# Performance work log

Hardware: AMD Instinct MI355X
Metric: run time of the kernel (lower is better)

The kernel has to match this reference:

```python
import jax, jax.numpy as jnp
import numpy as np

HIDDEN = 1000
DICT = 4811
T = 44
B = 256


def _lstm_cell(x, h, c, W_ih, W_hh, b_ih, b_hh):
    # gates: [B, 4*H], PyTorch order i, f, g, o
    gates = x @ W_ih.T + b_ih + h @ W_hh.T + b_hh
    i, f, g, o = jnp.split(gates, 4, axis=-1)
    i = jax.nn.sigmoid(i)
    f = jax.nn.sigmoid(f)
    g = jnp.tanh(g)
    o = jax.nn.sigmoid(o)
    c_new = f * c + i * g
    h_new = o * jnp.tanh(c_new)
    return h_new, c_new


def setup_inputs() -> dict:
    key = jax.random.key(0)
    ks = jax.random.split(key, 20)
    s = 0.02
    H = HIDDEN
    return {
        "x": jax.random.normal(ks[0], (B, T, H), jnp.float32),
        "h1": jax.random.normal(ks[1], (B, H), jnp.float32),
        "h2": jax.random.normal(ks[2], (B, H), jnp.float32),
        "c1": jax.random.normal(ks[3], (B, H), jnp.float32),
        "c2": jax.random.normal(ks[4], (B, H), jnp.float32),
        "layer_W": jax.random.normal(ks[5], (H, H), jnp.float32) * s,
        "layer_b": jnp.zeros((H,), jnp.float32),
        "W_ih1": jax.random.normal(ks[6], (4 * H, 2 * H), jnp.float32) * s,
        "W_hh1": jax.random.normal(ks[7], (4 * H, H), jnp.float32) * s,
        "b_ih1": jnp.zeros((4 * H,), jnp.float32),
        "b_hh1": jnp.zeros((4 * H,), jnp.float32),
        "W_ih2": jax.random.normal(ks[8], (4 * H, DICT + 2 * H), jnp.float32) * s,
        "W_hh2": jax.random.normal(ks[9], (4 * H, H), jnp.float32) * s,
        "b_ih2": jnp.zeros((4 * H,), jnp.float32),
        "b_hh2": jnp.zeros((4 * H,), jnp.float32),
        "out_W": jax.random.normal(ks[10], (DICT, H), jnp.float32) * s,
        "out_b": jnp.zeros((DICT,), jnp.float32),
    }


def reference(x, h1, h2, c1, c2, layer_W, layer_b,
              W_ih1, W_hh1, b_ih1, b_hh1,
              W_ih2, W_hh2, b_ih2, b_hh2,
              out_W, out_b):
    # input projection: [B, T, H]
    xp = x @ layer_W.T + layer_b
    prev0 = jnp.zeros((x.shape[0], DICT), x.dtype)

    def step(carry, xt):
        h1, c1, h2, c2, prev = carry
        l1_in = jnp.concatenate([xt, h1], axis=1)            # [B, 2H]
        h1n, c1n = _lstm_cell(l1_in, h1, c1, W_ih1, W_hh1, b_ih1, b_hh1)
        l2_in = jnp.concatenate([prev, h2, h1n], axis=1)     # [B, DICT+2H]
        h2n, c2n = _lstm_cell(l2_in, h2, c2, W_ih2, W_hh2, b_ih2, b_hh2)
        logits = h2n @ out_W.T + out_b                       # [B, DICT]
        # NOTE: original torch code softmaxes over dim=0 (batch axis)
        y = jax.nn.softmax(logits, axis=0)
        return (h1n, c1n, h2n, c2n, y), y

    xs = jnp.transpose(xp, (1, 0, 2))                        # [T, B, H]
    _, ys = jax.lax.scan(step, (h1, c1, h2, c2, prev0), xs)
    return jnp.transpose(ys, (1, 0, 2))                      # [B, T, DICT]
```

## Files before the change

### kernel.cpp

```cpp
#include <hip/hip_runtime.h>
#include <hip/hip_bf16.h>

#define HID   1000
#define DICT  4811
#define TT    44
#define BB    256
#define G4    4000
#define G4P   4096
#define K1P   2048
#define K2P   6912
#define HP    1024
#define DP    4864
#define Z2_H2 4864
#define Z2_H1 5888

typedef __attribute__((ext_vector_type(8))) short short8;
typedef __attribute__((ext_vector_type(4))) float f32x4;

__device__ __forceinline__ short f2b(float f) {
    unsigned u = __float_as_uint(f);
    unsigned r = (u + 0x7FFFu + ((u >> 16) & 1u)) >> 16;
    return (short)r;
}

__device__ __forceinline__ void gload16(const void* g, const short* l) {
    __builtin_amdgcn_global_load_lds(
        (const __attribute__((address_space(1))) unsigned int*)g,
        (__attribute__((address_space(3))) unsigned int*)l, 16, 0, 0);
}

__global__ void prep_w1p(const float* __restrict__ wih1, const float* __restrict__ whh1,
                         short* __restrict__ w) {
    for (size_t i = (size_t)blockIdx.x * blockDim.x + threadIdx.x; i < (size_t)G4P * K1P;
         i += (size_t)gridDim.x * blockDim.x) {
        int n = (int)(i >> 11), j = (int)(i & 2047);
        float v = 0.f;
        if (n < G4) {
            if (j < HID) v = wih1[(size_t)n * 2000 + j];
            else if (j >= 1024 && j < 1024 + HID) {
                int jj = j - 1024;
                v = wih1[(size_t)n * 2000 + HID + jj] + whh1[(size_t)n * HID + jj];
            }
        }
        w[i] = f2b(v);
    }
}

__global__ void prep_w2p(const float* __restrict__ wih2, const float* __restrict__ whh2,
                         short* __restrict__ w) {
    int n = blockIdx.y;
    int j = blockIdx.x * 256 + threadIdx.x;
    float v = 0.f;
    if (n < G4) {
        if (j < DICT) v = wih2[(size_t)n * 6811 + j];
        else if (j >= Z2_H2 && j < Z2_H2 + HID) {
            int jj = j - Z2_H2;
            v = wih2[(size_t)n * 6811 + DICT + jj] + whh2[(size_t)n * HID + jj];
        } else if (j >= Z2_H1 && j < Z2_H1 + HID) {
            int jj = j - Z2_H1;
            v = wih2[(size_t)n * 6811 + DICT + HID + jj];
        }
    }
    w[(size_t)n * K2P + j] = f2b(v);
}

__global__ void prep_outwp(const float* __restrict__ outw, short* __restrict__ w) {
    int n = blockIdx.y;
    int j = blockIdx.x * 256 + threadIdx.x;
    float v = (n < DICT && j < HID) ? outw[(size_t)n * HID + j] : 0.f;
    w[(size_t)n * HP + j] = f2b(v);
}

__global__ void prep_cvt(const float* __restrict__ src, short* __restrict__ dst, size_t n) {
    for (size_t i = (size_t)blockIdx.x * blockDim.x + threadIdx.x; i < n;
         i += (size_t)gridDim.x * blockDim.x)
        dst[i] = f2b(src[i]);
}

__global__ void prep_addv(const float* __restrict__ a, const float* __restrict__ b,
                          float* __restrict__ dst, int n) {
    int i = blockIdx.x * blockDim.x + threadIdx.x;
    if (i < n) dst[i] = a[i] + b[i];
}

__global__ void init_vec(const float* __restrict__ src, short* __restrict__ dst, int ld) {
    int i = blockIdx.x * blockDim.x + threadIdx.x;
    if (i >= BB * HID) return;
    int b = i / HID, h = i % HID;
    dst[(size_t)b * ld + h] = f2b(src[i]);
}

template <int EPI, int AF32>
__global__ __launch_bounds__(256) void gemm_nt(
    const void* __restrict__ Ap, int lda,
    const short* __restrict__ Bp, int ldb,
    const float* __restrict__ bias,
    void* __restrict__ Cp, long long partStride, int ldc,
    int M, int N, int Kvalid)
{
    __shared__ short As[64][40];
    __shared__ short Bs[64][40];
    const int tid  = threadIdx.x;
    const int lane = tid & 63;
    const int wave = tid >> 6;
    const int wm = wave >> 1, wn = wave & 1;
    const int tm = blockIdx.y * 64, tn = blockIdx.x * 64;
    const int srow = tid >> 2;
    const int scol = (tid & 3) * 8;

    const int nk = (Kvalid + 31) >> 5;
    const int s0 = (int)(((long long)nk * blockIdx.z) / gridDim.z);
    const int s1 = (int)(((long long)nk * (blockIdx.z + 1)) / gridDim.z);

    const int arow = tm + srow;
    const int brow = tn + srow;
    const bool bvalid = brow < N;

    auto loadA = [&](int ks) -> short8 {
        int k = (ks << 5) + scol;
        short8 r = {0, 0, 0, 0, 0, 0, 0, 0};
        if (k + 8 <= Kvalid) {
            if (AF32) {
                const f32x4* p = (const f32x4*)((const float*)Ap + (size_t)arow * lda + k);
                f32x4 u0 = p[0], u1 = p[1];
                r[0] = f2b(u0[0]); r[1] = f2b(u0[1]); r[2] = f2b(u0[2]); r[3] = f2b(u0[3]);
                r[4] = f2b(u1[0]); r[5] = f2b(u1[1]); r[6] = f2b(u1[2]); r[7] = f2b(u1[3]);
            } else {
                r = *(const short8*)((const short*)Ap + (size_t)arow * lda + k);
            }
        }
        return r;
    };
    auto loadB = [&](int ks) -> short8 {
        int k = (ks << 5) + scol;
        short8 r = {0, 0, 0, 0, 0, 0, 0, 0};
        if (bvalid && (k + 8 <= Kvalid))
            r = *(const short8*)(Bp + (size_t)brow * ldb + k);
        return r;
    };

    f32x4 acc[2][2];
    for (int a = 0; a < 2; ++a)
        for (int b = 0; b < 2; ++b)
            acc[a][b] = (f32x4){0.f, 0.f, 0.f, 0.f};

    short8 ra = loadA(s0), rb = loadB(s0);
    *(short8*)&As[srow][scol] = ra;
    *(short8*)&Bs[srow][scol] = rb;
    __syncthreads();

    const int kg = (lane >> 4) * 8;
    const int fr = lane & 15;

    for (int s = s0; s < s1; ++s) {
        short8 a0 = *(short8*)&As[wm * 32 + fr][kg];
        short8 a1 = *(short8*)&As[wm * 32 + 16 + fr][kg];
        short8 b0 = *(short8*)&Bs[wn * 32 + fr][kg];
        short8 b1 = *(short8*)&Bs[wn * 32 + 16 + fr][kg];
        short8 na, nb;
        if (s + 1 < s1) { na = loadA(s + 1); nb = loadB(s + 1); }
        acc[0][0] = __builtin_amdgcn_mfma_f32_16x16x32_bf16(a0, b0, acc[0][0], 0, 0, 0);
        acc[0][1] = __builtin_amdgcn_mfma_f32_16x16x32_bf16(a0, b1, acc[0][1], 0, 0, 0);
        acc[1][0] = __builtin_amdgcn_mfma_f32_16x16x32_bf16(a1, b0, acc[1][0], 0, 0, 0);
        acc[1][1] = __builtin_amdgcn_mfma_f32_16x16x32_bf16(a1, b1, acc[1][1], 0, 0, 0);
        __syncthreads();
        if (s + 1 < s1) {
            *(short8*)&As[srow][scol] = na;
            *(short8*)&Bs[srow][scol] = nb;
        }
        __syncthreads();
    }

    float* Cf = (float*)Cp + (size_t)partStride * blockIdx.z;
    for (int mi = 0; mi < 2; ++mi)
        for (int ni = 0; ni < 2; ++ni) {
            int col = tn + wn * 32 + ni * 16 + (lane & 15);
            if (col >= N) continue;
            float bv = bias ? bias[col] : 0.f;
            int row0 = tm + wm * 32 + mi * 16 + ((lane >> 4) << 2);
            f32x4 v = acc[mi][ni];
            for (int j = 0; j < 4; ++j) {
                int row = row0 + j;
                float val = v[j] + bv;
                if (EPI == 0) {
                    Cf[(size_t)row * ldc + col] = val;
                } else {
                    int b = row / TT, t = row % TT;
                    ((short*)Cp)[((size_t)t * BB + b) * ldc + col] = f2b(val);
                }
            }
        }
}

__global__ __launch_bounds__(512) void gemm_step(
    const short* __restrict__ A0, const short* __restrict__ A1, int splitK, int lda,
    const short* __restrict__ Bw, int ldb,
    float* __restrict__ C, long long partStride, int ldc, int nk)
{
    __shared__ __align__(16) short smem[2][10240];
    const int tid  = threadIdx.x;
    const int lane = tid & 63;
    const int w    = tid >> 6;
    const int wm = w >> 1, wn = w & 1;
    const int tn = blockIdx.x * 64;
    const int s0 = (int)(((long long)nk * blockIdx.z) / gridDim.z);
    const int s1 = (int)(((long long)nk * (blockIdx.z + 1)) / gridDim.z);

    const int sA0 = w * 128 + lane;
    const int sA1 = sA0 + 64;
    const int rA0 = sA0 >> 2, rA1 = sA1 >> 2;
    const size_t aoff0 = (size_t)rA0 * lda + (((sA0 & 3) ^ ((rA0 >> 1) & 3)) << 3);
    const size_t aoff1 = (size_t)rA1 * lda + (((sA1 & 3) ^ ((rA1 >> 1) & 3)) << 3);
    const bool doB = (w < 4);
    const int sB = w * 64 + lane;
    const int rB = sB >> 2;
    const size_t boff = (size_t)(tn + rB) * ldb + (((sB & 3) ^ ((rB >> 1) & 3)) << 3);

    auto stage = [&](int buf, int s) {
        const int k0 = s << 5;
        const short* As = (k0 < splitK) ? A0 : A1;
        const short* lA = &smem[buf][0];
        gload16(As + k0 + aoff0, lA + w * 1024);
        gload16(As + k0 + aoff1, lA + w * 1024 + 512);
        if (doB) gload16(Bw + k0 + boff, lA + 8192 + w * 512);
    };

    const int fr  = lane & 15;
    const int kgs = ((lane >> 4) << 3) ^ (((lane >> 1) & 3) << 3);
    const int aRd = (wm * 64 + fr) * 32 + kgs;
    const int bRd = 8192 + (wn * 32 + fr) * 32 + kgs;

    f32x4 acc[4][2];
    #pragma unroll
    for (int a = 0; a < 4; ++a)
        #pragma unroll
        for (int b = 0; b < 2; ++b)
            acc[a][b] = (f32x4){0.f, 0.f, 0.f, 0.f};

    stage(0, s0);
    __syncthreads();
    int cur = 0;
    for (int s = s0; s < s1; ++s) {
        if (s + 1 < s1) stage(cur ^ 1, s + 1);
        const short* bp = &smem[cur][0];
        short8 a0 = *(const short8*)(bp + aRd);
        short8 a1 = *(const short8*)(bp + aRd + 512);
        short8 a2 = *(const short8*)(bp + aRd + 1024);
        short8 a3 = *(const short8*)(bp + aRd + 1536);
        short8 b0 = *(const short8*)(bp + bRd);
        short8 b1 = *(const short8*)(bp + bRd + 512);
        acc[0][0] = __builtin_amdgcn_mfma_f32_16x16x32_bf16(a0, b0, acc[0][0], 0, 0, 0);
        acc[1][0] = __builtin_amdgcn_mfma_f32_16x16x32_bf16(a1, b0, acc[1][0], 0, 0, 0);
        acc[2][0] = __builtin_amdgcn_mfma_f32_16x16x32_bf16(a2, b0, acc[2][0], 0, 0, 0);
        acc[3][0] = __builtin_amdgcn_mfma_f32_16x16x32_bf16(a3, b0, acc[3][0], 0, 0, 0);
        acc[0][1] = __builtin_amdgcn_mfma_f32_16x16x32_bf16(a0, b1, acc[0][1], 0, 0, 0);
        acc[1][1] = __builtin_amdgcn_mfma_f32_16x16x32_bf16(a1, b1, acc[1][1], 0, 0, 0);
        acc[2][1] = __builtin_amdgcn_mfma_f32_16x16x32_bf16(a2, b1, acc[2][1], 0, 0, 0);
        acc[3][1] = __builtin_amdgcn_mfma_f32_16x16x32_bf16(a3, b1, acc[3][1], 0, 0, 0);
        __syncthreads();
        cur ^= 1;
    }

    float* Cp = C + (size_t)partStride * blockIdx.z;
    const int colb = tn + wn * 32 + fr;
    const int rowb = wm * 64 + ((lane >> 4) << 2);
    #pragma unroll
    for (int mi = 0; mi < 4; ++mi)
        #pragma unroll
        for (int ni = 0; ni < 2; ++ni) {
            int col = colb + ni * 16;
            int row0 = rowb + mi * 16;
            #pragma unroll
            for (int j = 0; j < 4; ++j)
                Cp[(size_t)(row0 + j) * ldc + col] = acc[mi][ni][j];
        }
}

__global__ void lstm_ew4(const float* __restrict__ g, long long ps,
                         const float* __restrict__ bias, float* __restrict__ c,
                         short* __restrict__ d1, int ld1,
                         short* __restrict__ d2, int ld2)
{
    int i = blockIdx.x * blockDim.x + threadIdx.x;
    if (i >= BB * HID) return;
    int b = i / HID, h = i % HID;
    size_t base = (size_t)b * G4P + h;
    float gi = bias[h], gf = bias[HID + h], gg = bias[2 * HID + h], go = bias[3 * HID + h];
    #pragma unroll
    for (int p = 0; p < 4; ++p) {
        const float* gp = g + (size_t)ps * p + base;
        gi += gp[0];
        gf += gp[HID];
        gg += gp[2 * HID];
        go += gp[3 * HID];
    }
    float ii = 1.f / (1.f + expf(-gi));
    float ff = 1.f / (1.f + expf(-gf));
    float tg = tanhf(gg);
    float oo = 1.f / (1.f + expf(-go));
    float cn = ff * c[i] + ii * tg;
    c[i] = cn;
    float hn = oo * tanhf(cn);
    short hb = f2b(hn);
    d1[(size_t)b * ld1 + h] = hb;
    d2[(size_t)b * ld2 + h] = hb;
}

__global__ __launch_bounds__(256) void softmax3(
    const float* __restrict__ lg, long long ps, const float* __restrict__ outb,
    float* __restrict__ out, short* __restrict__ z2, int t)
{
    __shared__ float red[8][32];
    const int dl = threadIdx.x & 31;
    const int bg = threadIdx.x >> 5;
    const int d = blockIdx.x * 32 + dl;
    const bool valid = d < DICT;
    float v[32];
    float m = -1e30f;
    if (valid) {
        const float bv = outb[d];
        #pragma unroll
        for (int i = 0; i < 32; ++i) {
            size_t o = (size_t)(bg * 32 + i) * DP + d;
            float x = lg[o] + lg[ps + o] + lg[2 * ps + o] + bv;
            v[i] = x;
            m = fmaxf(m, x);
        }
    } else {
        #pragma unroll
        for (int i = 0; i < 32; ++i) v[i] = 0.f;
    }
    red[bg][dl] = m;
    __syncthreads();
    m = red[0][dl];
    #pragma unroll
    for (int r = 1; r < 8; ++r) m = fmaxf(m, red[r][dl]);
    float s = 0.f;
    #pragma unroll
    for (int i = 0; i < 32; ++i) { v[i] = expf(v[i] - m); s += v[i]; }
    __syncthreads();
    red[bg][dl] = s;
    __syncthreads();
    s = 0.f;
    #pragma unroll
    for (int r = 0; r < 8; ++r) s += red[r][dl];
    const float inv = 1.f / s;
    if (valid) {
        #pragma unroll
        for (int i = 0; i < 32; ++i) {
            int b = bg * 32 + i;
            float y = v[i] * inv;
            out[(size_t)b * ((size_t)TT * DICT) + (size_t)t * DICT + d] = y;
            z2[(size_t)b * K2P + d] = f2b(y);
        }
    }
}

extern "C" void kernel_launch(void* const* d_in, const int* in_sizes, int n_in,
                              void* d_out, int out_size, void* d_ws, size_t ws_size,
                              hipStream_t stream)
{
    const float* x    = (const float*)d_in[0];
    const float* h1   = (const float*)d_in[1];
    const float* h2   = (const float*)d_in[2];
    const float* c1in = (const float*)d_in[3];
    const float* c2in = (const float*)d_in[4];
    const float* layW = (const float*)d_in[5];
    const float* layb = (const float*)d_in[6];
    const float* Wih1 = (const float*)d_in[7];
    const float* Whh1 = (const float*)d_in[8];
    const float* bih1 = (const float*)d_in[9];
    const float* bhh1 = (const float*)d_in[10];
    const float* Wih2 = (const float*)d_in[11];
    const float* Whh2 = (const float*)d_in[12];
    const float* bih2 = (const float*)d_in[13];
    const float* bhh2 = (const float*)d_in[14];
    const float* outW = (const float*)d_in[15];
    const float* outb = (const float*)d_in[16];
    float* out = (float*)d_out;
    (void)in_sizes; (void)n_in; (void)out_size; (void)ws_size;

    char* ws = (char*)d_ws;
    size_t off = 0;
    auto alloc = [&](size_t bytes) -> void* {
        size_t p = off;
        off = (off + bytes + 255) & ~(size_t)255;
        return (void*)(ws + p);
    };

    short* w1cat = (short*)alloc((size_t)G4P * K1P * 2);
    short* w2cat = (short*)alloc((size_t)G4P * K2P * 2);
    short* outwb = (short*)alloc((size_t)DP * HP * 2);
    short* laywb = (short*)alloc((size_t)HID * HID * 2);
    short* xp    = (short*)alloc((size_t)TT * BB * HP * 2);
    short* h1pad = (short*)alloc((size_t)BB * HP * 2);
    short* h2pad = (short*)alloc((size_t)BB * HP * 2);
    short* z2    = (short*)alloc((size_t)BB * K2P * 2);
    float* gbuf  = (float*)alloc((size_t)4 * BB * G4P * 4);
    float* lgtp  = (float*)alloc((size_t)3 * BB * DP * 4);
    float* c1    = (float*)alloc((size_t)BB * HID * 4);
    float* c2    = (float*)alloc((size_t)BB * HID * 4);
    float* bias1 = (float*)alloc((size_t)G4 * 4);
    float* bias2 = (float*)alloc((size_t)G4 * 4);

    hipMemsetAsync(xp, 0, (size_t)TT * BB * HP * 2, stream);
    hipMemsetAsync(z2, 0, (size_t)BB * K2P * 2, stream);
    hipMemsetAsync(h1pad, 0, (size_t)BB * HP * 2, stream);
    hipMemsetAsync(h2pad, 0, (size_t)BB * HP * 2, stream);

    prep_w1p<<<4096, 256, 0, stream>>>(Wih1, Whh1, w1cat);
    prep_w2p<<<dim3(27, G4P), 256, 0, stream>>>(Wih2, Whh2, w2cat);
    prep_outwp<<<dim3(4, DP), 256, 0, stream>>>(outW, outwb);
    prep_cvt<<<1024, 256, 0, stream>>>(layW, laywb, (size_t)HID * HID);
    prep_addv<<<16, 256, 0, stream>>>(bih1, bhh1, bias1, G4);
    prep_addv<<<16, 256, 0, stream>>>(bih2, bhh2, bias2, G4);
    init_vec<<<1000, 256, 0, stream>>>(h1, h1pad, HP);
    init_vec<<<1000, 256, 0, stream>>>(h2, h2pad, HP);
    init_vec<<<1000, 256, 0, stream>>>(h2, z2 + Z2_H2, K2P);
    hipMemcpyAsync(c1, c1in, (size_t)BB * HID * 4, hipMemcpyDeviceToDevice, stream);
    hipMemcpyAsync(c2, c2in, (size_t)BB * HID * 4, hipMemcpyDeviceToDevice, stream);

    gemm_nt<1, 1><<<dim3(16, (BB * TT) / 64, 1), 256, 0, stream>>>(
        x, HID, laywb, HID, layb, xp, 0, HP, BB * TT, HID, HID);

    const long long GP = (long long)BB * G4P;
    const long long LP = (long long)BB * DP;

    for (int t = 0; t < TT; ++t) {
        gemm_step<<<dim3(64, 1, 4), 512, 0, stream>>>(
            xp + (size_t)t * BB * HP, h1pad - HP, HP, HP, w1cat, K1P, gbuf, GP, G4P, K1P / 32);
        lstm_ew4<<<1000, 256, 0, stream>>>(gbuf, GP, bias1, c1, z2 + Z2_H1, K2P, h1pad, HP);

        gemm_step<<<dim3(64, 1, 4), 512, 0, stream>>>(
            z2, z2, 0, K2P, w2cat, K2P, gbuf, GP, G4P, K2P / 32);
        lstm_ew4<<<1000, 256, 0, stream>>>(gbuf, GP, bias2, c2, z2 + Z2_H2, K2P, h2pad, HP);

        gemm_step<<<dim3(76, 1, 3), 512, 0, stream>>>(
            h2pad, h2pad, 0, HP, outwb, HP, lgtp, LP, DP, HP / 32);

        softmax3<<<151, 256, 0, stream>>>(lgtp, LP, outb, out, z2, t);
    }
}
```

Baseline: 4.155 ms.

## Use 3-stage pipelined 128-wide GEMM tiles with rebalanced split-K per step

Replaces the double-buffered 256x64 step GEMM with a triple-buffered 256x128 tile. It uses explicit vmcnt waits and barriers so global-to-LDS loads run ahead of the MFMA work. The grids are rebalanced: fewer N blocks and more split-K partitions (8 for the layer-2 GEMM, 4 for the output GEMM), with the elementwise and softmax kernels templated on the number of partials they reduce. Each wave now does a 4x4 MFMA block for more reuse per LDS read, at the cost of more registers, larger LDS use and more partial-sum traffic to global memory.

Result: faster. 3.510 ms (-15.5%).

```diff
diff --git a/kernel.cpp b/kernel.cpp
--- a/kernel.cpp
+++ b/kernel.cpp
@@ -13,6 +13,7 @@
 #define DP    4864
 #define Z2_H2 4864
 #define Z2_H1 5888
+#define PD    3
 
 typedef __attribute__((ext_vector_type(8))) short short8;
 typedef __attribute__((ext_vector_type(4))) float f32x4;
@@ -192,82 +193,98 @@
         }
 }
 
-__global__ __launch_bounds__(512) void gemm_step(
-    const short* __restrict__ A0, const short* __restrict__ A1, int splitK, int lda,
+__global__ __launch_bounds__(512) void gemm_step3(
+    const short* __restrict__ A0, const short* __restrict__ A1, int splitA, int lda,
     const short* __restrict__ Bw, int ldb,
     float* __restrict__ C, long long partStride, int ldc, int nk)
 {
-    __shared__ __align__(16) short smem[2][10240];
+    __shared__ __align__(16) short smem[PD][12288];
     const int tid  = threadIdx.x;
     const int lane = tid & 63;
     const int w    = tid >> 6;
     const int wm = w >> 1, wn = w & 1;
-    const int tn = blockIdx.x * 64;
+    const int tn = blockIdx.x * 128;
     const int s0 = (int)(((long long)nk * blockIdx.z) / gridDim.z);
     const int s1 = (int)(((long long)nk * (blockIdx.z + 1)) / gridDim.z);
 
-    const int sA0 = w * 128 + lane;
-    const int sA1 = sA0 + 64;
-    const int rA0 = sA0 >> 2, rA1 = sA1 >> 2;
-    const size_t aoff0 = (size_t)rA0 * lda + (((sA0 & 3) ^ ((rA0 >> 1) & 3)) << 3);
-    const size_t aoff1 = (size_t)rA1 * lda + (((sA1 & 3) ^ ((rA1 >> 1) & 3)) << 3);
-    const bool doB = (w < 4);
-    const int sB = w * 64 + lane;
-    const int rB = sB >> 2;
-    const size_t boff = (size_t)(tn + rB) * ldb + (((sB & 3) ^ ((rB >> 1) & 3)) << 3);
+    const int cA0 = w * 64 + lane;
+    const int cA1 = cA0 + 512;
+    const int rA0 = cA0 >> 2, rA1 = cA1 >> 2;
+    const size_t aoff0 = (size_t)rA0 * lda + (size_t)((((cA0 & 3) ^ ((rA0 >> 1) & 3))) << 3);
+    const size_t aoff1 = (size_t)rA1 * lda + (size_t)((((cA1 & 3) ^ ((rA1 >> 1) & 3))) << 3);
+    const int cB = w * 64 + lane;
+    const int rB = cB >> 2;
+    const size_t boff = (size_t)(tn + rB) * ldb + (size_t)((((cB & 3) ^ ((rB >> 1) & 3))) << 3);
 
     auto stage = [&](int buf, int s) {
         const int k0 = s << 5;
-        const short* As = (k0 < splitK) ? A0 : A1;
-        const short* lA = &smem[buf][0];
-        gload16(As + k0 + aoff0, lA + w * 1024);
-        gload16(As + k0 + aoff1, lA + w * 1024 + 512);
-        if (doB) gload16(Bw + k0 + boff, lA + 8192 + w * 512);
+        const short* As = (k0 < splitA) ? A0 : A1;
+        const short* l = &smem[buf][0];
+        gload16(As + k0 + aoff0, l + w * 512);
+        gload16(As + k0 + aoff1, l + 4096 + w * 512);
+        gload16(Bw + k0 + boff,  l + 8192 + w * 512);
     };
 
-    const int fr  = lane & 15;
-    const int kgs = ((lane >> 4) << 3) ^ (((lane >> 1) & 3) << 3);
-    const int aRd = (wm * 64 + fr) * 32 + kgs;
-    const int bRd = 8192 + (wn * 32 + fr) * 32 + kgs;
-
-    f32x4 acc[4][2];
+    const int fr = lane & 15;
+    const int kg = lane >> 4;
+    int aRd[4], bRd[4];
+    #pragma unroll
+    for (int mi = 0; mi < 4; ++mi) {
+        int row = wm * 64 + mi * 16 + fr;
+        aRd[mi] = row * 32 + ((kg ^ ((row >> 1) & 3)) << 3);
+    }
+    #pragma unroll
+    for (int ni = 0; ni < 4; ++ni) {
+        int row = wn * 64 + ni * 16 + fr;
+        bRd[ni] = 8192 + row * 32 + ((kg ^ ((row >> 1) & 3)) << 3);
+    }
+
+    f32x4 acc[4][4];
     #pragma unroll
     for (int a = 0; a < 4; ++a)
         #pragma unroll
-        for (int b = 0; b < 2; ++b)
+        for (int b = 0; b < 4; ++b)
             acc[a][b] = (f32x4){0.f, 0.f, 0.f, 0.f};
 
-    stage(0, s0);
-    __syncthreads();
-    int cur = 0;
+    #pragma unroll
+    for (int i = 0; i < PD; ++i)
+        if (s0 + i < s1) stage(i, s0 + i);
+
+    int buf = 0;
     for (int s = s0; s < s1; ++s) {
-        if (s + 1 < s1) stage(cur ^ 1, s + 1);
-        const short* bp = &smem[cur][0];
-        short8 a0 = *(const short8*)(bp + aRd);
-        short8 a1 = *(const short8*)(bp + aRd + 512);
-        short8 a2 = *(const short8*)(bp + aRd + 1024);
-        short8 a3 = *(const short8*)(bp + aRd + 1536);
-        short8 b0 = *(const short8*)(bp + bRd);
-        short8 b1 = *(const short8*)(bp + bRd + 512);
-        acc[0][0] = __builtin_amdgcn_mfma_f32_16x16x32_bf16(a0, b0, acc[0][0], 0, 0, 0);
-        acc[1][0] = __builtin_amdgcn_mfma_f32_16x16x32_bf16(a1, b0, acc[1][0], 0, 0, 0);
-        acc[2][0] = __builtin_amdgcn_mfma_f32_16x16x32_bf16(a2, b0, acc[2][0], 0, 0, 0);
-        acc[3][0] = __builtin_amdgcn_mfma_f32_16x16x32_bf16(a3, b0, acc[3][0], 0, 0, 0);
-        acc[0][1] = __builtin_amdgcn_mfma_f32_16x16x32_bf16(a0, b1, acc[0][1], 0, 0, 0);
-        acc[1][1] = __builtin_amdgcn_mfma_f32_16x16x32_bf16(a1, b1, acc[1][1], 0, 0, 0);
-        acc[2][1] = __builtin_amdgcn_mfma_f32_16x16x32_bf16(a2, b1, acc[2][1], 0, 0, 0);
-        acc[3][1] = __builtin_amdgcn_mfma_f32_16x16x32_bf16(a3, b1, acc[3][1], 0, 0, 0);
-        __syncthreads();
-        cur ^= 1;
+        const int ahead = s1 - 1 - s;
+        if (ahead >= 2)      asm volatile("s_waitcnt vmcnt(6)" ::: "memory");
+        else if (ahead == 1) asm volatile("s_waitcnt vmcnt(3)" ::: "memory");
+        else                 asm volatile("s_waitcnt vmcnt(0)" ::: "memory");
+        __builtin_amdgcn_s_barrier();
+
+        const short* bp = &smem[buf][0];
+        short8 af[4], bf[4];
+        #pragma unroll
+        for (int i = 0; i < 4; ++i) af[i] = *(const short8*)(bp + aRd[i]);
+        #pragma unroll
+        for (int i = 0; i < 4; ++i) bf[i] = *(const short8*)(bp + bRd[i]);
+        asm volatile("s_waitcnt lgkmcnt(0)" ::: "memory");
+        __builtin_amdgcn_sched_barrier(0);
+        __builtin_amdgcn_s_barrier();
+        if (s + PD < s1) stage(buf, s + PD);
+
+        #pragma unroll
+        for (int mi = 0; mi < 4; ++mi)
+            #pragma unroll
+            for (int ni = 0; ni < 4; ++ni)
+                acc[mi][ni] = __builtin_amdgcn_mfma_f32_16x16x32_bf16(af[mi], bf[ni], acc[mi][ni], 0, 0, 0);
+
+        buf = (buf + 1 == PD) ? 0 : buf + 1;
     }
 
     float* Cp = C + (size_t)partStride * blockIdx.z;
-    const int colb = tn + wn * 32 + fr;
-    const int rowb = wm * 64 + ((lane >> 4) << 2);
+    const int colb = tn + wn * 64 + fr;
+    const int rowb = wm * 64 + (kg << 2);
     #pragma unroll
     for (int mi = 0; mi < 4; ++mi)
         #pragma unroll
-        for (int ni = 0; ni < 2; ++ni) {
+        for (int ni = 0; ni < 4; ++ni) {
             int col = colb + ni * 16;
             int row0 = rowb + mi * 16;
             #pragma unroll
@@ -276,7 +293,8 @@
         }
 }
 
-__global__ void lstm_ew4(const float* __restrict__ g, long long ps,
+template <int NP>
+__global__ void lstm_ewN(const float* __restrict__ g, long long ps,
                          const float* __restrict__ bias, float* __restrict__ c,
                          short* __restrict__ d1, int ld1,
                          short* __restrict__ d2, int ld2)
@@ -287,7 +305,7 @@
     size_t base = (size_t)b * G4P + h;
     float gi = bias[h], gf = bias[HID + h], gg = bias[2 * HID + h], go = bias[3 * HID + h];
     #pragma unroll
-    for (int p = 0; p < 4; ++p) {
+    for (int p = 0; p < NP; ++p) {
         const float* gp = g + (size_t)ps * p + base;
         gi += gp[0];
         gf += gp[HID];
@@ -306,7 +324,8 @@
     d2[(size_t)b * ld2 + h] = hb;
 }
 
-__global__ __launch_bounds__(256) void softmax3(
+template <int NP>
+__global__ __launch_bounds__(256) void softmaxN(
     const float* __restrict__ lg, long long ps, const float* __restrict__ outb,
     float* __restrict__ out, short* __restrict__ z2, int t)
 {
@@ -322,7 +341,9 @@
         #pragma unroll
         for (int i = 0; i < 32; ++i) {
             size_t o = (size_t)(bg * 32 + i) * DP + d;
-            float x = lg[o] + lg[ps + o] + lg[2 * ps + o] + bv;
+            float x = bv;
+            #pragma unroll
+            for (int p = 0; p < NP; ++p) x += lg[(size_t)ps * p + o];
             v[i] = x;
             m = fmaxf(m, x);
         }
@@ -396,8 +417,8 @@
     short* h1pad = (short*)alloc((size_t)BB * HP * 2);
     short* h2pad = (short*)alloc((size_t)BB * HP * 2);
     short* z2    = (short*)alloc((size_t)BB * K2P * 2);
-    float* gbuf  = (float*)alloc((size_t)4 * BB * G4P * 4);
-    float* lgtp  = (float*)alloc((size_t)3 * BB * DP * 4);
+    float* gbuf  = (float*)alloc((size_t)8 * BB * G4P * 4);
+    float* lgtp  = (float*)alloc((size_t)4 * BB * DP * 4);
     float* c1    = (float*)alloc((size_t)BB * HID * 4);
     float* c2    = (float*)alloc((size_t)BB * HID * 4);
     float* bias1 = (float*)alloc((size_t)G4 * 4);
@@ -427,17 +448,17 @@
     const long long LP = (long long)BB * DP;
 
     for (int t = 0; t < TT; ++t) {
-        gemm_step<<<dim3(64, 1, 4), 512, 0, stream>>>(
-            xp + (size_t)t * BB * HP, h1pad - HP, HP, HP, w1cat, K1P, gbuf, GP, G4P, K1P / 32);
-        lstm_ew4<<<1000, 256, 0, stream>>>(gbuf, GP, bias1, c1, z2 + Z2_H1, K2P, h1pad, HP);
-
-        gemm_step<<<dim3(64, 1, 4), 512, 0, stream>>>(
+        gemm_step3<<<dim3(32, 1, 4), 512, 0, stream>>>(
+            xp + (size_t)t * BB * HP, h1pad - HP, 1024, HP, w1cat, K1P, gbuf, GP, G4P, K1P / 32);
+        lstm_ewN<4><<<1000, 256, 0, stream>>>(gbuf, GP, bias1, c1, z2 + Z2_H1, K2P, h1pad, HP);
+
+        gemm_step3<<<dim3(32, 1, 8), 512, 0, stream>>>(
             z2, z2, 0, K2P, w2cat, K2P, gbuf, GP, G4P, K2P / 32);
-        lstm_ew4<<<1000, 256, 0, stream>>>(gbuf, GP, bias2, c2, z2 + Z2_H2, K2P, h2pad, HP);
-
-        gemm_step<<<dim3(76, 1, 3), 512, 0, stream>>>(
+        lstm_ewN<8><<<1000, 256, 0, stream>>>(gbuf, GP, bias2, c2, z2 + Z2_H2, K2P, h2pad, HP);
+
+        gemm_step3<<<dim3(38, 1, 4), 512, 0, stream>>>(
             h2pad, h2pad, 0, HP, outwb, HP, lgtp, LP, DP, HP / 32);
 
-        softmax3<<<151, 256, 0, stream>>>(lgtp, LP, outb, out, z2, t);
-    }
-}
+        softmaxN<4><<<151, 256, 0, stream>>>(lgtp, LP, outb, out, z2, t);
+    }
+}
```
